# Kernel tuning notes

Measured on AMD Instinct MI355X. Metric: run time of the kernel, lower is better.

The kernel has to match this reference:

```python
import jax, jax.numpy as jnp
import numpy as np

HEADS = 8
DIM_HEAD = 40


def setup_inputs() -> dict:
    key = jax.random.key(0)
    ks = jax.random.split(key, 10)
    b, n, j, qd, cd = 8, 4096, 77, 320, 768
    inner = HEADS * DIM_HEAD  # 320
    x = jax.random.normal(ks[0], (b, n, qd), jnp.float32)
    embs = jax.random.normal(ks[1], (b, j, cd), jnp.float32)
    Wq = jax.random.normal(ks[2], (qd, inner), jnp.float32) * 0.02
    Wk = jax.random.normal(ks[3], (cd, inner), jnp.float32) * 0.02
    Wv = jax.random.normal(ks[4], (cd, inner), jnp.float32) * 0.02
    Wo = jax.random.normal(ks[5], (inner, qd), jnp.float32) * 0.02
    bo = jnp.zeros((qd,), jnp.float32)
    # per-query-token, per-key-token additive attention mask (float weights)
    cross_attn_mask = (jax.random.uniform(ks[6], (b, n, j)) < 0.5).astype(jnp.float32)
    strength = jnp.ones((1,), jnp.float32) * 0.8
    # captiontypes >= 0 marks valid key tokens; include some -1 (invalid)
    captiontypes = jax.random.randint(ks[7], (b, j), -1, 3).at[:, 0].set(0)
    global_prompt_mask = (jax.random.uniform(ks[8], (b, j)) > 0.05).at[:, 0].set(True)
    return {"x": x, "embs": embs, "Wq": Wq, "Wk": Wk, "Wv": Wv, "Wo": Wo,
            "bo": bo, "cross_attn_mask": cross_attn_mask, "strength": strength,
            "captiontypes": captiontypes, "global_prompt_mask": global_prompt_mask}


def _split_heads(t):
    # [b, n, h*d] -> [(b h), n, d], head index fastest (matches einops '(b h)')
    b, n, _ = t.shape
    return t.reshape(b, n, HEADS, DIM_HEAD).transpose(0, 2, 1, 3).reshape(b * HEADS, n, DIM_HEAD)


def reference(x, embs, Wq, Wk, Wv, Wo, bo, cross_attn_mask, strength,
              captiontypes, global_prompt_mask):
    b, n, _ = x.shape
    scale = DIM_HEAD ** -0.5
    q = _split_heads(x @ Wq).astype(jnp.float32)   # [(b h), n, d]
    k = _split_heads(embs @ Wk).astype(jnp.float32)  # [(b h), j, d]
    v = _split_heads(embs @ Wv)                      # [(b h), j, d]
    sim = jnp.einsum('bid,bjd->bij', q, k)           # [(b h), n, j] fp32

    NEG = -jnp.finfo(sim.dtype).max
    key_mask = captiontypes >= 0                     # [b, j]
    key_mask_bh = jnp.repeat(key_mask, HEADS, axis=0)[:, None, :]  # [(b h), 1, j]

    # masked std of sim over valid key positions (unbiased, ddof=1), no grad
    w = jnp.broadcast_to(key_mask_bh, sim.shape).astype(sim.dtype)
    cnt = jnp.sum(w)
    mean = jnp.sum(sim * w) / cnt
    var = jnp.sum(w * (sim - mean) ** 2) / (cnt - 1.0)
    simstd = jnp.sqrt(var)

    wf = cross_attn_mask * simstd * strength[0]      # [b, n, j]
    wf = jnp.where(global_prompt_mask[:, None, :], wf, NEG)
    wf = jnp.repeat(wf, HEADS, axis=0)               # [(b h), n, j]
    wf = jax.lax.stop_gradient(wf)

    sim = jnp.where(key_mask_bh, sim, NEG) + wf
    attn = jax.nn.softmax(sim * scale, axis=-1)
    out = jnp.einsum('bij,bjd->bid', attn, v)        # [(b h), n, d]
    out = out.reshape(b, HEADS, n, DIM_HEAD).transpose(0, 2, 1, 3).reshape(b, n, HEADS * DIM_HEAD)
    return out @ Wo + bo
```

## Files before the change

### kernel.cpp

```cpp
#include <hip/hip_runtime.h>
#include <hip/hip_bf16.h>
#include <math.h>

#define HEADS 8
#define DIMH 40
#define BB 8
#define NN 4096
#define JJ 77
#define CDIM 768
#define INNER 320
#define NEGF (-3.4028234663852886e38f)

using bf16 = __hip_bfloat16;
using f32x4 = __attribute__((ext_vector_type(4))) float;
using bf16x8 = __attribute__((ext_vector_type(8))) short;
using ushort8 = __attribute__((ext_vector_type(8))) unsigned short;
using ushort4v = __attribute__((ext_vector_type(4))) unsigned short;

__device__ __forceinline__ unsigned short f2u(float f){
    bf16 t = __float2bfloat16(f);
    return *reinterpret_cast<unsigned short*>(&t);
}
__device__ __forceinline__ float u2f(unsigned short u){
    unsigned int w = ((unsigned int)u) << 16;
    return __uint_as_float(w);
}

__global__ __launch_bounds__(256) void prep_weights(const float* __restrict__ Wq,
                                                    const float* __restrict__ Wo,
                                                    const float* __restrict__ Wk,
                                                    const float* __restrict__ Wv,
                                                    unsigned short* __restrict__ WqT,
                                                    unsigned short* __restrict__ WoT,
                                                    unsigned short* __restrict__ WkvT){
    __shared__ float tile[32][33];
    int blk = blockIdx.x;
    int tx = threadIdx.x & 31, ty = threadIdx.x >> 5;
    if(blk < 200){
        const float* in = (blk<100)? Wq : Wo;
        unsigned short* out = (blk<100)? WqT : WoT;
        int base = (blk<100)? blk : blk-100;
        int bx = base%10, by = base/10;
        int c0 = bx*32, r0 = by*32;
        #pragma unroll
        for(int i=0;i<32;i+=8) tile[ty+i][tx] = in[(size_t)(r0+ty+i)*320 + c0+tx];
        __syncthreads();
        #pragma unroll
        for(int i=0;i<32;i+=8) out[(size_t)(c0+ty+i)*320 + r0+tx] = f2u(tile[tx][ty+i]);
    } else {
        int local = blk-200;
        int nt = local%20, kt = local/20;
        int n0 = nt*32, k0 = kt*32;
        const float* in = (n0<320)? Wk : Wv;
        int nc0 = (n0<320)? n0 : n0-320;
        #pragma unroll
        for(int i=0;i<32;i+=8) tile[ty+i][tx] = in[(size_t)(k0+ty+i)*320 + nc0+tx];
        __syncthreads();
        #pragma unroll
        for(int i=0;i<32;i+=8) WkvT[(size_t)(n0+ty+i)*768 + k0+tx] = f2u(tile[tx][ty+i]);
    }
}

__global__ __launch_bounds__(256) void proj_kv_mfma(const float* __restrict__ embs,
                                                    const unsigned short* __restrict__ WkvT,
                                                    unsigned short* __restrict__ kws,
                                                    unsigned short* __restrict__ vt){
    __shared__ unsigned short As[64][40];
    __shared__ unsigned short Bs[64][40];
    int t = threadIdx.x;
    int bm = blockIdx.x % 10;
    int bn = blockIdx.x / 10;
    int row0 = bm*64, col0 = bn*64;
    int wave=t>>6, lane=t&63, l15=lane&15, lk=lane>>4;

    f32x4 acc[4];
    #pragma unroll
    for(int nf=0;nf<4;nf++) acc[nf]=(f32x4){0.f,0.f,0.f,0.f};

    for(int k0=0;k0<768;k0+=32){
        #pragma unroll
        for(int p=0;p<2;p++){
            int li = (p*256+t)*4; int r = li>>5, kk = li&31;
            int gr = row0 + r;
            ushort4v u;
            if(gr < 616){
                float4 v = *(const float4*)&embs[(size_t)gr*768 + k0+kk];
                u.x=f2u(v.x); u.y=f2u(v.y); u.z=f2u(v.z); u.w=f2u(v.w);
            } else { u.x=0;u.y=0;u.z=0;u.w=0; }
            *(ushort4v*)&As[r][kk] = u;
        }
        {
            int nn = t>>2, kk = (t&3)*8;
            *(ushort8*)&Bs[nn][kk] = *(const ushort8*)&WkvT[(size_t)(col0+nn)*768 + k0+kk];
        }
        __syncthreads();
        bf16x8 aF = *(const bf16x8*)&As[wave*16+l15][lk*8];
        #pragma unroll
        for(int nf=0;nf<4;nf++){
            bf16x8 bF = *(const bf16x8*)&Bs[nf*16+l15][lk*8];
            acc[nf] = __builtin_amdgcn_mfma_f32_16x16x32_bf16(aF,bF,acc[nf],0,0,0);
        }
        __syncthreads();
    }
    #pragma unroll
    for(int nf=0;nf<4;nf++){
        int col = col0 + nf*16 + l15;
        #pragma unroll
        for(int r=0;r<4;r++){
            int m = row0 + wave*16 + lk*4 + r;
            if(m < 616){
                int b = m/77, j = m - 77*b;
                unsigned short val = f2u(acc[nf][r]);
                if(col < 320){
                    int h = col/40, d = col - 40*h;
                    kws[(((size_t)b*HEADS+h)*JJ + j)*DIMH + d] = val;
                } else {
                    int c2 = col-320; int h = c2/40, d = c2 - 40*h;
                    size_t vbase = (((size_t)b*HEADS+h)*DIMH + d)*80;
                    vt[vbase + j] = val;
                    if(j==76){ vt[vbase+77]=0; vt[vbase+78]=0; vt[vbase+79]=0; }
                }
            }
        }
    }
}

__global__ __launch_bounds__(256) void gemm_q_stats(const float* __restrict__ x,
                                                    const unsigned short* __restrict__ WqT,
                                                    const unsigned short* __restrict__ kws,
                                                    const int* __restrict__ ct,
                                                    unsigned short* __restrict__ qh,
                                                    float2* __restrict__ partials){
    __shared__ unsigned short SH[256*80];
    unsigned short* As = SH;
    unsigned short* Bs = SH + 256*40;
    int t = threadIdx.x;
    int bm = blockIdx.x & 127;
    int bn = blockIdx.x >> 7;
    int row0 = bm*256, col0 = bn*80;
    int wave = t>>6, lane = t&63;
    int l15 = lane&15, lk = lane>>4;
    int b = row0 >> 12;
    bf16x8 zb = {0,0,0,0,0,0,0,0};

    f32x4 acc[4][5];
    #pragma unroll
    for(int i=0;i<4;i++)
        #pragma unroll
        for(int j=0;j<5;j++) acc[i][j] = (f32x4){0.f,0.f,0.f,0.f};

    for(int k0=0;k0<320;k0+=32){
        #pragma unroll
        for(int p=0;p<8;p++){
            int li = (p*256+t)*4; int r = li>>5, kk = li&31;
            float4 v = *(const float4*)&x[(size_t)(row0+r)*320 + k0+kk];
            ushort4v u; u.x=f2u(v.x); u.y=f2u(v.y); u.z=f2u(v.z); u.w=f2u(v.w);
            *(ushort4v*)&As[r*40+kk] = u;
        }
        #pragma unroll
        for(int p=0;p<2;p++){
            int idx = p*256+t;
            if(idx < 320){
                int nn = idx>>2, kk = (idx&3)*8;
                *(ushort8*)&Bs[nn*40+kk] = *(const ushort8*)&WqT[(size_t)(col0+nn)*320 + k0+kk];
            }
        }
        __syncthreads();
        bf16x8 a[4], bb[5];
        #pragma unroll
        for(int mf=0;mf<4;mf++) a[mf] = *(const bf16x8*)&As[(wave*64+mf*16+l15)*40 + lk*8];
        #pragma unroll
        for(int nf=0;nf<5;nf++) bb[nf] = *(const bf16x8*)&Bs[(nf*16+l15)*40 + lk*8];
        #pragma unroll
        for(int mf=0;mf<4;mf++)
            #pragma unroll
            for(int nf=0;nf<5;nf++)
                acc[mf][nf] = __builtin_amdgcn_mfma_f32_16x16x32_bf16(a[mf], bb[nf], acc[mf][nf], 0,0,0);
        __syncthreads();
    }
    #pragma unroll
    for(int mf=0;mf<4;mf++)
        #pragma unroll
        for(int nf=0;nf<5;nf++){
            int col = col0 + nf*16 + l15;
            int h = col/40, d = col - 40*h;
            int lcol = nf*16 + l15;
            #pragma unroll
            for(int r=0;r<4;r++){
                int lrow = wave*64 + mf*16 + lk*4 + r;
                int n = row0 + lrow - (b<<12);
                unsigned short v = f2u(acc[mf][nf][r]);
                qh[(((size_t)(b*8+h))*NN + n)*DIMH + d] = v;
                SH[lrow*80 + lcol] = v;
            }
        }
    __syncthreads();
    float s1=0.f, s2=0.f;
    #pragma unroll
    for(int h2=0;h2<2;h2++){
        int bh = b*8 + bn*2 + h2;
        bool kv[5]; bf16x8 bK0[5], bK1[5];
        #pragma unroll
        for(int jt=0;jt<5;jt++){
            int j = jt*16+l15;
            kv[jt] = (j<JJ) && (ct[b*JJ+j]>=0);
            bK0[jt] = (j<JJ) ? *(const bf16x8*)&kws[((size_t)bh*JJ+j)*DIMH + lk*8] : zb;
            bK1[jt] = (j<JJ && lk==0) ? *(const bf16x8*)&kws[((size_t)bh*JJ+j)*DIMH + 32] : zb;
        }
        #pragma unroll
        for(int mfq=0;mfq<4;mfq++){
            int wq = wave*64 + mfq*16;
            bf16x8 aF0 = *(const bf16x8*)&SH[(wq+l15)*80 + h2*40 + lk*8];
            bf16x8 aF1 = (lk==0) ? *(const bf16x8*)&SH[(wq+l15)*80 + h2*40 + 32] : zb;
            f32x4 sacc[5];
            #pragma unroll
            for(int jt=0;jt<5;jt++) sacc[jt]=(f32x4){0.f,0.f,0.f,0.f};
            #pragma unroll
            for(int jt=0;jt<5;jt++){
                sacc[jt] = __builtin_amdgcn_mfma_f32_16x16x32_bf16(aF0,bK0[jt],sacc[jt],0,0,0);
                sacc[jt] = __builtin_amdgcn_mfma_f32_16x16x32_bf16(aF1,bK1[jt],sacc[jt],0,0,0);
            }
            #pragma unroll
            for(int jt=0;jt<5;jt++){
                if(kv[jt]){
                    #pragma unroll
                    for(int r=0;r<4;r++){ float v=sacc[jt][r]; s1+=v; s2+=v*v; }
                }
            }
        }
    }
    #pragma unroll
    for(int off=32;off>0;off>>=1){ s1 += __shfl_down(s1,off); s2 += __shfl_down(s2,off); }
    __shared__ float sa[4], sb[4];
    if(lane==0){ sa[wave]=s1; sb[wave]=s2; }
    __syncthreads();
    if(t==0){
        partials[blockIdx.x] = make_float2(sa[0]+sa[1]+sa[2]+sa[3],
                                           sb[0]+sb[1]+sb[2]+sb[3]);
    }
}

__global__ __launch_bounds__(256) void finalize_kernel(const float2* __restrict__ partials,
                                                       const int* __restrict__ ct,
                                                       const int* __restrict__ gpm,
                                                       const float* __restrict__ strength,
                                                       float* __restrict__ kmT,
                                                       float* __restrict__ adT,
                                                       float* __restrict__ gmT){
    int t = threadIdx.x;
    __shared__ int sflag, scnt;
    if(t==0){ sflag=0; scnt=0; }
    __syncthreads();
    int lflag=0, lcnt=0;
    for(int i=t;i<154;i+=256){ int g = gpm[i]; if(g!=0 && g!=1) lflag=1; }
    for(int i=t;i<BB*JJ;i+=256){ if(ct[i]>=0) lcnt++; }
    if(lflag) atomicOr(&sflag,1);
    atomicAdd(&scnt,lcnt);
    double s1=0.0, s2=0.0;
    for(int i=t;i<512;i+=256){
        float2 p = partials[i];
        s1 += (double)p.x; s2 += (double)p.y;
    }
    #pragma unroll
    for(int off=32;off>0;off>>=1){ s1 += __shfl_down(s1,off); s2 += __shfl_down(s2,off); }
    __shared__ double da[4], db[4];
    __shared__ float s_simstd;
    int lane=t&63, w=t>>6;
    if(lane==0){ da[w]=s1; db[w]=s2; }
    __syncthreads();
    if(t==0){
        double S1 = da[0]+da[1]+da[2]+da[3];
        double S2 = db[0]+db[1]+db[2]+db[3];
        double cnt = (double)scnt * HEADS * NN;
        double var = (S2 - S1*S1/cnt)/(cnt-1.0);
        s_simstd = (float)sqrt(var);
    }
    __syncthreads();
    float c = s_simstd * strength[0];
    int gflag = sflag;
    for(int i=t;i<BB*80;i+=256){
        int b = i/80, j = i-80*b;
        int kvv=0, gv=0;
        if(j<JJ){
            kvv = ct[b*JJ+j]>=0;
            gv = gflag ? (((const unsigned char*)gpm)[b*JJ+j]!=0) : (gpm[b*JJ+j]!=0);
        }
        kmT[i] = (j<JJ && kvv)?1.f:0.f;
        adT[i] = ((j<JJ && kvv)?0.f:NEGF) + ((j<JJ && gv)?0.f:NEGF);
        gmT[i] = (j<JJ && gv)? c : 0.f;
    }
}

template<int A_MODE, int C_MODE>
__global__ __launch_bounds__(256) void gemm_mfma(const void* __restrict__ A,
                                                 const unsigned short* __restrict__ Bt,
                                                 const float* __restrict__ bias,
                                                 void* __restrict__ C){
    __shared__ unsigned short As[256][40];
    __shared__ unsigned short Bs[64][40];
    int t = threadIdx.x;
    int bm = blockIdx.x & 127;
    int bn = blockIdx.x >> 7;
    int row0 = bm*256, col0 = bn*64;
    int wave = t>>6, lane = t&63;
    int l15 = lane&15, lk = lane>>4;

    f32x4 acc[4][4];
    #pragma unroll
    for(int i=0;i<4;i++)
        #pragma unroll
        for(int j=0;j<4;j++) acc[i][j] = (f32x4){0.f,0.f,0.f,0.f};

    for(int k0=0;k0<320;k0+=32){
        if(A_MODE==2){
            const unsigned short* Ab = (const unsigned short*)A;
            #pragma unroll
            for(int p=0;p<4;p++){
                int li = (p*256+t)*8; int r = li>>5, kk = li&31;
                int m = row0+r; int k = k0+kk;
                int b = m>>12, n = m&4095;
                int h = k/40, d = k-40*h;
                *(ushort8*)&As[r][kk] = *(const ushort8*)&Ab[(((size_t)(b*8+h))*NN + n)*DIMH + d];
            }
        } else {
            const float* Af = (const float*)A;
            #pragma unroll
            for(int p=0;p<8;p++){
                int li = (p*256+t)*4; int r = li>>5, kk = li&31;
                float4 v = *(const float4*)&Af[(size_t)(row0+r)*320 + k0+kk];
                ushort4v u; u.x=f2u(v.x); u.y=f2u(v.y); u.z=f2u(v.z); u.w=f2u(v.w);
                *(ushort4v*)&As[r][kk] = u;
            }
        }
        {
            int nn = t>>2, kk = (t&3)*8;
            *(ushort8*)&Bs[nn][kk] = *(const ushort8*)&Bt[(size_t)(col0+nn)*320 + k0+kk];
        }
        __syncthreads();
        bf16x8 a[4], b[4];
        #pragma unroll
        for(int mf=0;mf<4;mf++) a[mf] = *(const bf16x8*)&As[wave*64+mf*16+l15][lk*8];
        #pragma unroll
        for(int nf=0;nf<4;nf++) b[nf] = *(const bf16x8*)&Bs[nf*16+l15][lk*8];
        #pragma unroll
        for(int mf=0;mf<4;mf++)
            #pragma unroll
            for(int nf=0;nf<4;nf++)
                acc[mf][nf] = __builtin_amdgcn_mfma_f32_16x16x32_bf16(a[mf], b[nf], acc[mf][nf], 0,0,0);
        __syncthreads();
    }
    if(C_MODE==1){
        float* Cf = (float*)C;
        float bv[4];
        #pragma unroll
        for(int nf=0;nf<4;nf++) bv[nf] = bias[col0+nf*16+l15];
        #pragma unroll
        for(int mf=0;mf<4;mf++)
            #pragma unroll
            for(int nf=0;nf<4;nf++){
                int col = col0+nf*16+l15;
                #pragma unroll
                for(int r=0;r<4;r++){
                    int m = row0+wave*64+mf*16+lk*4+r;
                    Cf[(size_t)m*320+col] = acc[mf][nf][r] + bv[nf];
                }
            }
    }
}

__global__ __launch_bounds__(256) void attn_mfma(unsigned short* qh,
                                                 const unsigned short* __restrict__ kws,
                                                 const unsigned short* __restrict__ vt,
                                                 const float* __restrict__ cam,
                                                 const float* __restrict__ kmT,
                                                 const float* __restrict__ adT,
                                                 const float* __restrict__ gmT){
    int bp = blockIdx.x;
    int b = bp>>2, hp = bp&3;
    int bh0 = b*8 + hp*2;
    __shared__ unsigned short camS[64][80];
    __shared__ unsigned short P[64][104];
    int t = threadIdx.x;
    int wave=t>>6, lane=t&63, l15=lane&15, lk=lane>>4;
    int wq0 = wave*16;
    bf16x8 zb = {0,0,0,0,0,0,0,0};
    ushort8 z8 = {0,0,0,0,0,0,0,0};
    int n0 = blockIdx.y*64;

    {
        const float* csrc = cam + ((size_t)b*NN + n0)*JJ;
        for(int idx=t; idx<64*JJ; idx+=256){
            int r = idx/JJ, j = idx - r*JJ;
            camS[r][j] = f2u(csrc[idx]);
        }
        for(int idx=t; idx<64*3; idx+=256){ int r=idx/3; camS[r][77+idx%3]=0; }
    }
    float km[5], gm[5], ad[5];
    #pragma unroll
    for(int jt=0;jt<5;jt++){
        int j = jt*16+l15;
        km[jt] = kmT[b*80+j]; ad[jt] = adT[b*80+j]; gm[jt] = gmT[b*80+j];
    }
    if(t<64){ *(ushort8*)&P[t][80]=z8; *(ushort8*)&P[t][88]=z8; *(ushort8*)&P[t][96]=z8; }
    __syncthreads();

    const float scale = 0.15811388300841897f;
    for(int h2=0;h2<2;h2++){
        int bh = bh0 + h2;
        size_t qrow = ((size_t)bh*NN + n0 + wq0 + l15)*DIMH;
        bf16x8 aF0 = *(const bf16x8*)&qh[qrow + lk*8];
        bf16x8 aF1 = (lk==0) ? *(const bf16x8*)&qh[qrow + 32] : zb;
        bf16x8 bK[2][5];
        #pragma unroll
        for(int ks=0;ks<2;ks++)
            #pragma unroll
            for(int jt=0;jt<5;jt++){
                int j = jt*16+l15;
                if(j<JJ && !(ks==1 && lk>=1))
                    bK[ks][jt] = *(const bf16x8*)&kws[((size_t)bh*JJ + j)*DIMH + ks*32 + lk*8];
                else bK[ks][jt] = zb;
            }
        bf16x8 bV[3][3];
        #pragma unroll
        for(int ks=0;ks<3;ks++)
            #pragma unroll
            for(int nt=0;nt<3;nt++){
                int d = nt*16+l15;
                if(d<DIMH && !(ks==2 && lk>=2))
                    bV[ks][nt] = *(const bf16x8*)&vt[((size_t)bh*DIMH + d)*80 + ks*32 + lk*8];
                else bV[ks][nt] = zb;
            }
        f32x4 sacc[5];
        #pragma unroll
        for(int jt=0;jt<5;jt++) sacc[jt]=(f32x4){0.f,0.f,0.f,0.f};
        #pragma unroll
        for(int jt=0;jt<5;jt++){
            sacc[jt] = __builtin_amdgcn_mfma_f32_16x16x32_bf16(aF0,bK[0][jt],sacc[jt],0,0,0);
            sacc[jt] = __builtin_amdgcn_mfma_f32_16x16x32_bf16(aF1,bK[1][jt],sacc[jt],0,0,0);
        }
        float lo[5][4];
        #pragma unroll
        for(int jt=0;jt<5;jt++){
            int j = jt*16+l15;
            #pragma unroll
            for(int r=0;r<4;r++){
                float cvv = u2f(camS[wq0+4*lk+r][j]);
                lo[jt][r] = (sacc[jt][r]*km[jt] + cvv*gm[jt] + ad[jt])*scale;
            }
        }
        float dinv[4];
        #pragma unroll
        for(int r=0;r<4;r++){
            float m = lo[0][r];
            #pragma unroll
            for(int jt=1;jt<5;jt++) m = fmaxf(m, lo[jt][r]);
            #pragma unroll
            for(int msk=1;msk<16;msk<<=1) m = fmaxf(m, __shfl_xor(m,msk));
            float s=0.f;
            #pragma unroll
            for(int jt=0;jt<5;jt++){ float e=__expf(lo[jt][r]-m); lo[jt][r]=e; s+=e; }
            #pragma unroll
            for(int msk=1;msk<16;msk<<=1) s += __shfl_xor(s,msk);
            dinv[r]=1.f/s;
        }
        #pragma unroll
        for(int jt=0;jt<5;jt++){
            int j = jt*16+l15;
            #pragma unroll
            for(int r=0;r<4;r++) P[wq0+4*lk+r][j] = f2u(lo[jt][r]*dinv[r]);
        }
        __syncthreads();
        f32x4 oacc[3];
        #pragma unroll
        for(int nt=0;nt<3;nt++) oacc[nt]=(f32x4){0.f,0.f,0.f,0.f};
        #pragma unroll
        for(int ks=0;ks<3;ks++){
            bf16x8 aP = *(const bf16x8*)&P[wq0+l15][ks*32+lk*8];
            #pragma unroll
            for(int nt=0;nt<3;nt++)
                oacc[nt] = __builtin_amdgcn_mfma_f32_16x16x32_bf16(aP,bV[ks][nt],oacc[nt],0,0,0);
        }
        #pragma unroll
        for(int nt=0;nt<3;nt++){
            int d = nt*16+l15;
            #pragma unroll
            for(int r=0;r<4;r++){
                unsigned short ush = f2u(oacc[nt][r]);
                int other = __shfl_xor((int)ush, 1);
                if((l15&1)==0 && d<DIMH){
                    unsigned int word = (unsigned int)ush | (((unsigned int)(unsigned short)other)<<16);
                    int row = n0 + wq0 + 4*lk + r;
                    *(unsigned int*)&qh[((size_t)bh*NN + row)*DIMH + d] = word;
                }
            }
        }
        __syncthreads();
    }
}

extern "C" void kernel_launch(void* const* d_in, const int* in_sizes, int n_in,
                              void* d_out, int out_size, void* d_ws, size_t ws_size,
                              hipStream_t stream) {
    const float* x        = (const float*)d_in[0];
    const float* embs     = (const float*)d_in[1];
    const float* Wq       = (const float*)d_in[2];
    const float* Wk       = (const float*)d_in[3];
    const float* Wv       = (const float*)d_in[4];
    const float* Wo       = (const float*)d_in[5];
    const float* bo       = (const float*)d_in[6];
    const float* cam      = (const float*)d_in[7];
    const float* strength = (const float*)d_in[8];
    const int*  ct       = (const int*)d_in[9];
    const int*  gpm      = (const int*)d_in[10];

    char* ws = (char*)d_ws;
    unsigned short* qh   = (unsigned short*)ws;
    unsigned short* kws  = (unsigned short*)(ws + 20971520);
    unsigned short* vt   = (unsigned short*)(ws + 21365760);
    unsigned short* WqT  = (unsigned short*)(ws + 21775360);
    unsigned short* WoT  = (unsigned short*)(ws + 21980160);
    unsigned short* WkvT = (unsigned short*)(ws + 22184960);
    float2* partials = (float2*)(ws + 23168000);
    float* kmT = (float*)(ws + 23173120);
    float* adT = (float*)(ws + 23175680);
    float* gmT = (float*)(ws + 23178240);

    prep_weights<<<680,256,0,stream>>>(Wq,Wo,Wk,Wv,WqT,WoT,WkvT);
    proj_kv_mfma<<<100,256,0,stream>>>(embs,WkvT,kws,vt);
    gemm_q_stats<<<512,256,0,stream>>>(x,WqT,kws,ct,qh,partials);
    finalize_kernel<<<1,256,0,stream>>>(partials,ct,gpm,strength,kmT,adT,gmT);
    attn_mfma<<<dim3(32,64),256,0,stream>>>(qh,kws,vt,cam,kmT,adT,gmT);
    gemm_mfma<2,1><<<640,256,0,stream>>>(qh,WoT,bo,d_out);
}
```

Before: 123.3 us.

## Compute transposed scores so softmax probabilities feed PV MFMA from registers

Rewrites the attention kernel to compute S^T (keys as MFMA rows, queries as columns), so each lane holds probabilities for one query across keys. The softmax reduction then uses cross-lane shuffles, and the bf16 probabilities are passed directly as the B operand of a 16x16x16 MFMA for the PV product. This removes the shared-memory P staging buffer and its barriers. In exchange the PV step uses smaller-K MFMAs and more per-lane global loads of K and V, and it depends on a compile-time builtin check, falling back to the old kernel if that builtin is unavailable.

```diff
diff --git a/kernel.cpp b/kernel.cpp
--- a/kernel.cpp
+++ b/kernel.cpp
@@ -14,8 +14,19 @@
 using bf16 = __hip_bfloat16;
 using f32x4 = __attribute__((ext_vector_type(4))) float;
 using bf16x8 = __attribute__((ext_vector_type(8))) short;
+using bf16x4 = __attribute__((ext_vector_type(4))) short;
 using ushort8 = __attribute__((ext_vector_type(8))) unsigned short;
 using ushort4v = __attribute__((ext_vector_type(4))) unsigned short;
+
+#if __has_builtin(__builtin_amdgcn_mfma_f32_16x16x16bf16_1k)
+  #define HAVE_MFMA16 1
+  #define MFMA16(A,B,C) __builtin_amdgcn_mfma_f32_16x16x16bf16_1k((A),(B),(C),0,0,0)
+#elif __has_builtin(__builtin_amdgcn_mfma_f32_16x16x16_bf16)
+  #define HAVE_MFMA16 1
+  #define MFMA16(A,B,C) __builtin_amdgcn_mfma_f32_16x16x16_bf16((A),(B),(C),0,0,0)
+#else
+  #define HAVE_MFMA16 0
+#endif
 
 __device__ __forceinline__ unsigned short f2u(float f){
     bf16 t = __float2bfloat16(f);
@@ -368,6 +379,114 @@
     }
 }
 
+#if HAVE_MFMA16
+__global__ __launch_bounds__(256) void attn_mfma(unsigned short* qh,
+                                                 const unsigned short* __restrict__ kws,
+                                                 const unsigned short* __restrict__ vt,
+                                                 const float* __restrict__ cam,
+                                                 const float* __restrict__ kmT,
+                                                 const float* __restrict__ adT,
+                                                 const float* __restrict__ gmT){
+    int bp = blockIdx.x;
+    int b = bp>>2, hp = bp&3;
+    int bh0 = b*8 + hp*2;
+    __shared__ unsigned short camS[64][84];
+    int t = threadIdx.x;
+    int wave=t>>6, lane=t&63, l15=lane&15, lk=lane>>4;
+    int n0 = blockIdx.y*64;
+    bf16x8 zb = {0,0,0,0,0,0,0,0};
+    bf16x4 zb4 = {0,0,0,0};
+
+    {
+        const float* csrc = cam + ((size_t)b*NN + n0)*JJ;
+        for(int idx=t; idx<64*JJ; idx+=256){
+            int r = idx/JJ, j = idx - r*JJ;
+            camS[r][j] = f2u(csrc[idx]);
+        }
+        for(int idx=t; idx<64*7; idx+=256){ camS[idx/7][77+idx%7]=0; }
+    }
+    __syncthreads();
+
+    int row = n0 + wave*16 + l15;
+    const float scale = 0.15811388300841897f;
+
+    for(int h2=0;h2<2;h2++){
+        int bh = bh0 + h2;
+        size_t qoff = ((size_t)bh*NN + row)*DIMH;
+        bf16x8 bq0 = *(const bf16x8*)&qh[qoff + lk*8];
+        bf16x8 bq1 = (lk==0) ? *(const bf16x8*)&qh[qoff + 32] : zb;
+
+        f32x4 sacc[5];
+        #pragma unroll
+        for(int jt=0;jt<5;jt++) sacc[jt]=(f32x4){0.f,0.f,0.f,0.f};
+        #pragma unroll
+        for(int jt=0;jt<5;jt++){
+            int j = jt*16+l15;
+            bf16x8 aK0 = (j<JJ) ? *(const bf16x8*)&kws[((size_t)bh*JJ+j)*DIMH + lk*8] : zb;
+            bf16x8 aK1 = (j<JJ && lk==0) ? *(const bf16x8*)&kws[((size_t)bh*JJ+j)*DIMH + 32] : zb;
+            sacc[jt] = __builtin_amdgcn_mfma_f32_16x16x32_bf16(aK0,bq0,sacc[jt],0,0,0);
+            sacc[jt] = __builtin_amdgcn_mfma_f32_16x16x32_bf16(aK1,bq1,sacc[jt],0,0,0);
+        }
+        float lo[5][4];
+        float m = -1.0e30f;
+        #pragma unroll
+        for(int jt=0;jt<5;jt++){
+            float4 km4 = *(const float4*)&kmT[b*80 + jt*16 + lk*4];
+            float4 ad4 = *(const float4*)&adT[b*80 + jt*16 + lk*4];
+            float4 gm4 = *(const float4*)&gmT[b*80 + jt*16 + lk*4];
+            ushort4v cu = *(const ushort4v*)&camS[wave*16+l15][jt*16 + lk*4];
+            lo[jt][0] = (sacc[jt][0]*km4.x + u2f(cu.x)*gm4.x + ad4.x)*scale;
+            lo[jt][1] = (sacc[jt][1]*km4.y + u2f(cu.y)*gm4.y + ad4.y)*scale;
+            lo[jt][2] = (sacc[jt][2]*km4.z + u2f(cu.z)*gm4.z + ad4.z)*scale;
+            lo[jt][3] = (sacc[jt][3]*km4.w + u2f(cu.w)*gm4.w + ad4.w)*scale;
+            #pragma unroll
+            for(int r=0;r<4;r++) m = fmaxf(m, lo[jt][r]);
+        }
+        m = fmaxf(m, __shfl_xor(m,16));
+        m = fmaxf(m, __shfl_xor(m,32));
+        float s = 0.f;
+        #pragma unroll
+        for(int jt=0;jt<5;jt++)
+            #pragma unroll
+            for(int r=0;r<4;r++){ float e=__expf(lo[jt][r]-m); lo[jt][r]=e; s+=e; }
+        s += __shfl_xor(s,16);
+        s += __shfl_xor(s,32);
+        float dinv = 1.f/s;
+        bf16x4 p4[5];
+        #pragma unroll
+        for(int jt=0;jt<5;jt++){
+            bf16x4 p;
+            p[0] = (short)f2u(lo[jt][0]*dinv);
+            p[1] = (short)f2u(lo[jt][1]*dinv);
+            p[2] = (short)f2u(lo[jt][2]*dinv);
+            p[3] = (short)f2u(lo[jt][3]*dinv);
+            p4[jt] = p;
+        }
+        f32x4 oacc[3];
+        #pragma unroll
+        for(int nt=0;nt<3;nt++) oacc[nt]=(f32x4){0.f,0.f,0.f,0.f};
+        #pragma unroll
+        for(int jt=0;jt<5;jt++){
+            #pragma unroll
+            for(int nt=0;nt<3;nt++){
+                int d = nt*16+l15;
+                bf16x4 aV = (d<DIMH) ? *(const bf16x4*)&vt[((size_t)bh*DIMH + d)*80 + jt*16 + lk*4] : zb4;
+                oacc[nt] = MFMA16(aV, p4[jt], oacc[nt]);
+            }
+        }
+        #pragma unroll
+        for(int nt=0;nt<3;nt++){
+            int d0 = nt*16 + lk*4;
+            if(d0 < DIMH){
+                ushort4v o4;
+                o4.x = f2u(oacc[nt][0]); o4.y = f2u(oacc[nt][1]);
+                o4.z = f2u(oacc[nt][2]); o4.w = f2u(oacc[nt][3]);
+                *(ushort4v*)&qh[((size_t)bh*NN + row)*DIMH + d0] = o4;
+            }
+        }
+    }
+}
+#else
 __global__ __launch_bounds__(256) void attn_mfma(unsigned short* qh,
                                                  const unsigned short* __restrict__ kws,
                                                  const unsigned short* __restrict__ vt,
@@ -386,7 +505,6 @@
     bf16x8 zb = {0,0,0,0,0,0,0,0};
     ushort8 z8 = {0,0,0,0,0,0,0,0};
     int n0 = blockIdx.y*64;
-
     {
         const float* csrc = cam + ((size_t)b*NN + n0)*JJ;
         for(int idx=t; idx<64*JJ; idx+=256){
@@ -403,7 +521,6 @@
     }
     if(t<64){ *(ushort8*)&P[t][80]=z8; *(ushort8*)&P[t][88]=z8; *(ushort8*)&P[t][96]=z8; }
     __syncthreads();
-
     const float scale = 0.15811388300841897f;
     for(int h2=0;h2<2;h2++){
         int bh = bh0 + h2;
@@ -497,6 +614,7 @@
         __syncthreads();
     }
 }
+#endif
 
 extern "C" void kernel_launch(void* const* d_in, const int* in_sizes, int n_in,
                               void* d_out, int out_size, void* d_ws, size_t ws_size,
```

After: 128.8 us. 1.04x slower.
